# Kernel tuning notes

Hardware: AMD Instinct MI355X
Metric: run time of the kernel (lower is better)

## Reference

```python
import jax, jax.numpy as jnp
import numpy as np

WS = 7
B, Dd, Hh, Wd, C, NH = 1, 28, 28, 28, 384, 12

def _rel_index(ws):
    coords = np.stack(np.meshgrid(np.arange(ws), np.arange(ws), np.arange(ws), indexing='ij'))
    cf = coords.reshape(3, -1)
    rel = (cf[:, :, None] - cf[:, None, :]).transpose(1, 2, 0) + (ws - 1)
    rel[:, :, 0] *= (2 * ws - 1) ** 2
    rel[:, :, 1] *= (2 * ws - 1)
    return rel.sum(-1)  # (ws^3, ws^3)

REL_IDX = _rel_index(WS)

def setup_inputs():
    key = jax.random.key(0)
    ks = jax.random.split(key, 8)
    L = Dd * Hh * Wd
    s = 0.02
    return {
        'skip': jax.random.normal(ks[0], (B, L, C), jnp.float32),
        'x_up': jax.random.normal(ks[1], (B, L, C), jnp.float32),
        'D': Dd, 'H': Hh, 'W': Wd,
        'ln1_g': jnp.ones((C,), jnp.float32), 'ln1_b': jnp.zeros((C,), jnp.float32),
        'kv_w': jax.random.normal(ks[2], (C, 2 * C), jnp.float32) * s,
        'kv_b': jnp.zeros((2 * C,), jnp.float32),
        'rpb': jax.random.normal(ks[3], ((2 * WS - 1) ** 3, NH), jnp.float32) * s,
        'proj_w': jax.random.normal(ks[4], (C, C), jnp.float32) * s,
        'proj_b': jnp.zeros((C,), jnp.float32),
        'ln2_g': jnp.ones((C,), jnp.float32), 'ln2_b': jnp.zeros((C,), jnp.float32),
        'mlp_w1': jax.random.normal(ks[5], (C, 4 * C), jnp.float32) * s,
        'mlp_b1': jnp.zeros((4 * C,), jnp.float32),
        'mlp_w2': jax.random.normal(ks[6], (4 * C, C), jnp.float32) * s,
        'mlp_b2': jnp.zeros((C,), jnp.float32),
    }

def _ln(x, g, b):
    m = jnp.mean(x, -1, keepdims=True)
    v = jnp.mean(jnp.square(x - m), -1, keepdims=True)
    return (x - m) * jax.lax.rsqrt(v + 1e-5) * g + b

def _win_part(x):
    b, d, h, w, c = x.shape
    x = x.reshape(b, d // WS, WS, h // WS, WS, w // WS, WS, c)
    return x.transpose(0, 1, 3, 5, 2, 4, 6, 7).reshape(-1, WS ** 3, c)

def _win_rev(x, b, d, h, w):
    c = x.shape[-1]
    x = x.reshape(b, d // WS, h // WS, w // WS, WS, WS, WS, c)
    return x.transpose(0, 1, 4, 2, 5, 3, 6, 7).reshape(b, d, h, w, c)

def reference(skip, x_up, D, H, W, ln1_g, ln1_b, kv_w, kv_b, rpb, proj_w, proj_b, ln2_g, ln2_b, mlp_w1, mlp_b1, mlp_w2, mlp_b2):
    b, L, c = skip.shape
    x = x_up + skip  # wrapper residual; shortcut of the inner block
    # inner block was built with shift_size=0 -> no cyclic shift, attn_mask unused
    sk = _win_part(_ln(skip, ln1_g, ln1_b).reshape(b, D, H, W, c))   # (nW, N, C) -> K,V source
    qx = _win_part(_ln(x_up, ln1_g, ln1_b).reshape(b, D, H, W, c))   # (nW, N, C) -> Q source
    nW, N, _ = sk.shape
    hd = c // NH
    kv = (sk @ kv_w + kv_b).reshape(nW, N, 2, NH, hd)
    k, v = kv[:, :, 0], kv[:, :, 1]                  # (nW, N, NH, hd)
    q = qx.reshape(nW, N, NH, hd) * (hd ** -0.5)     # no q projection in WindowAttention_kv
    attn = jnp.einsum('wqhd,wkhd->whqk', q, k)
    bias = rpb[REL_IDX.reshape(-1)].reshape(N, N, NH).transpose(2, 0, 1)
    attn = jax.nn.softmax(attn + bias[None], axis=-1)
    o = jnp.einsum('whqk,wkhd->wqhd', attn, v).reshape(nW, N, c)
    o = o @ proj_w + proj_b
    o = _win_rev(o, b, D, H, W).reshape(b, L, c)
    x = x + o
    h1 = jax.nn.gelu(_ln(x, ln2_g, ln2_b) @ mlp_w1 + mlp_b1)
    x = x + h1 @ mlp_w2 + mlp_b2
    return x
```

## Files before the change

### kernel.cpp

```cpp
#include <hip/hip_runtime.h>
#include <hip/hip_bf16.h>
#include <cstdint>

typedef unsigned short u16;
typedef short s16x8 __attribute__((ext_vector_type(8)));
typedef short s16x4 __attribute__((ext_vector_type(4)));
typedef float f32x4 __attribute__((ext_vector_type(4)));

#define C_DIM 384
#define NHEAD 12
#define HD    32
#define NTOK  343
#define NWIN  64
#define LTOT  21952
#define SIDE  28

__device__ __forceinline__ float u2f(u16 u) {
    return __uint_as_float(((unsigned int)u) << 16);
}
__device__ __forceinline__ u16 f2b(float f) {
    unsigned int u = __float_as_uint(f);
    return (u16)((u + 0x7fffu + ((u >> 16) & 1u)) >> 16);
}
__device__ __forceinline__ float exp2_hw(float x) {
    float r;
    asm("v_exp_f32 %0, %1" : "=v"(r) : "v"(x));
    return r;
}
__device__ __forceinline__ unsigned int pk_bf16(float lo, float hi) {
    unsigned int r;
    asm("v_cvt_pk_bf16_f32 %0, %1, %2" : "=v"(r) : "v"(lo), "v"(hi));
    return r;
}
__device__ __forceinline__ float gelu_fast(float x) {
    float e = exp2_hw(-2.3022083f * (x + 0.044715f * x * x * x));
    return x * __builtin_amdgcn_rcpf(1.f + e);
}
__device__ __forceinline__ void gl16(const u16* g, u16* l) {
    __builtin_amdgcn_global_load_lds(
        (const __attribute__((address_space(1))) void*)g,
        (__attribute__((address_space(3))) void*)l, 16, 0, 0);
}

__global__ __launch_bounds__(256) void k_wt(
    const float* __restrict__ W, u16* __restrict__ Wt, int K, int N)
{
    __shared__ float T[64][65];
    int k0 = blockIdx.x * 64, n0 = blockIdx.y * 64;
    int t = threadIdx.x;
    int c = t & 63, rg = t >> 6;
#pragma unroll
    for (int i = 0; i < 16; i++) {
        int r = rg * 16 + i;
        T[r][c] = W[(size_t)(k0 + r) * N + n0 + c];
    }
    __syncthreads();
    int k = t & 63, ng = t >> 6;
#pragma unroll
    for (int i = 0; i < 16; i++) {
        int n = ng * 16 + i;
        Wt[(size_t)(n0 + n) * K + k0 + k] = f2b(T[k][n]);
    }
}

__global__ __launch_bounds__(256) void k_wt_pi(
    const float* __restrict__ W, u16* __restrict__ Wt, int K, int N)
{
    __shared__ float T[64][65];
    int k0 = blockIdx.x * 64, n0 = blockIdx.y * 64;
    int t = threadIdx.x;
    int c = t & 63, rg = t >> 6;
#pragma unroll
    for (int i = 0; i < 16; i++) {
        int r = rg * 16 + i;
        T[r][c] = W[(size_t)(k0 + r) * N + n0 + c];
    }
    __syncthreads();
    int k = t & 63, ng = t >> 6;
    int kg = k0 + k;
    int j = kg & 127, ct = j >> 4, nn = j & 15;
    int kp = (kg & ~127) | ((ct >> 1) << 5) | (nn << 1) | (ct & 1);
#pragma unroll
    for (int i = 0; i < 16; i++) {
        int n = ng * 16 + i;
        Wt[(size_t)(n0 + n) * K + kp] = f2b(T[k][n]);
    }
}

__global__ __launch_bounds__(256) void k_bias(
    const float* __restrict__ rpb, u16* __restrict__ biasPl)
{
    int h = blockIdx.x, q = blockIdx.y;
    int qc = min(q, NTOK - 1);
    int qz = qc / 49, qrem = qc % 49, qy = qrem / 7, qx = qrem % 7;
    int cq = qz * 169 + qy * 13 + qx;
    u16* dst = biasPl + ((size_t)h * 352 + q) * 352;
    for (int k = threadIdx.x; k < 352; k += 256) {
        int kc = min(k, NTOK - 1);
        int kz = kc / 49, krem = kc % 49, ky = krem / 7, kx = krem % 7;
        int ck = kz * 169 + ky * 13 + kx;
        dst[k] = f2b(rpb[(size_t)(cq - ck + 1098) * NHEAD + h] * 1.4426950408889634f);
    }
}

#define QSCALE 0.2550348772f

__global__ __launch_bounds__(256) void k_lnprep(
    const float* __restrict__ skip, const float* __restrict__ xup,
    const float* __restrict__ g, const float* __restrict__ bta,
    u16* __restrict__ skW, u16* __restrict__ qW, u16* __restrict__ res)
{
    int t = blockIdx.x * 4 + (threadIdx.x >> 6);
    int lane = threadIdx.x & 63;
    const float* ps = skip + (size_t)t * C_DIM;
    const float* px = xup + (size_t)t * C_DIM;
    float vs[6], vx[6];
    float s1 = 0.f, s2 = 0.f, x1 = 0.f, x2 = 0.f;
#pragma unroll
    for (int j = 0; j < 6; j++) {
        float a = ps[lane + j * 64];
        float b = px[lane + j * 64];
        vs[j] = a; vx[j] = b;
        s1 += a; s2 += a * a; x1 += b; x2 += b * b;
    }
#pragma unroll
    for (int off = 32; off; off >>= 1) {
        s1 += __shfl_xor(s1, off);
        s2 += __shfl_xor(s2, off);
        x1 += __shfl_xor(x1, off);
        x2 += __shfl_xor(x2, off);
    }
    float ms = s1 * (1.f / 384.f), mx = x1 * (1.f / 384.f);
    float rs = rsqrtf(fmaxf(s2 * (1.f / 384.f) - ms * ms, 0.f) + 1e-5f);
    float rx = rsqrtf(fmaxf(x2 * (1.f / 384.f) - mx * mx, 0.f) + 1e-5f);
    int d = t / 784, rem = t % 784, hh = rem / 28, ww = rem % 28;
    int win = (d / 7) * 16 + (hh / 7) * 4 + (ww / 7);
    int n = (d % 7) * 49 + (hh % 7) * 7 + (ww % 7);
    size_t dst = ((size_t)(win * NTOK + n)) * C_DIM + lane;
    size_t td  = (size_t)t * C_DIM + lane;
#pragma unroll
    for (int j = 0; j < 6; j++) {
        int c = lane + j * 64;
        float gg = g[c], bb = bta[c];
        skW[dst + j * 64] = f2b((vs[j] - ms) * rs * gg + bb);
        qW[dst + j * 64]  = f2b(((vx[j] - mx) * rx * gg + bb) * QSCALE);
        res[td + j * 64]  = f2b(vs[j] + vx[j]);
    }
}

__global__ __launch_bounds__(256) void k_ln2(
    const u16* __restrict__ x2, const float* __restrict__ g,
    const float* __restrict__ bta, u16* __restrict__ lnx)
{
    int t = blockIdx.x * 4 + (threadIdx.x >> 6);
    int lane = threadIdx.x & 63;
    const u16* p = x2 + (size_t)t * C_DIM;
    float v[6];
    float s1 = 0.f, s2 = 0.f;
#pragma unroll
    for (int j = 0; j < 6; j++) {
        float a = u2f(p[lane + j * 64]);
        v[j] = a; s1 += a; s2 += a * a;
    }
#pragma unroll
    for (int off = 32; off; off >>= 1) {
        s1 += __shfl_xor(s1, off);
        s2 += __shfl_xor(s2, off);
    }
    float m = s1 * (1.f / 384.f);
    float r = rsqrtf(fmaxf(s2 * (1.f / 384.f) - m * m, 0.f) + 1e-5f);
    size_t dst = (size_t)t * C_DIM + lane;
#pragma unroll
    for (int j = 0; j < 6; j++) {
        int c = lane + j * 64;
        lnx[dst + j * 64] = f2b((v[j] - m) * r * g[c] + bta[c]);
    }
}

__device__ __forceinline__ void gemm128_gl(
    const u16* __restrict__ A, const u16* __restrict__ Bt, int K, int M,
    int rowBase, int colBase, int tid,
    u16 (*As)[32], u16 (*Bs)[32], f32x4 acc[4][4])
{
    const int sr  = tid >> 2;
    const int scg = (tid & 3) << 3;
    const int lane = tid & 63, wv = tid >> 6;
    const int m16 = lane & 15, quad = lane >> 4;
    const int wr = (wv >> 1) << 6, wc = (wv & 1) << 6;

    int ra0 = min(rowBase + sr, M - 1);
    int ra1 = min(rowBase + 64 + sr, M - 1);
    const u16* pa0 = A + (size_t)ra0 * K + scg;
    const u16* pa1 = A + (size_t)ra1 * K + scg;
    const u16* pb0 = Bt + (size_t)(colBase + sr) * K + scg;
    const u16* pb1 = Bt + (size_t)(colBase + 64 + sr) * K + scg;

    u16* a0d = &As[0][0]  + wv * 512;
    u16* a1d = &As[64][0] + wv * 512;
    u16* b0d = &Bs[0][0]  + wv * 512;
    u16* b1d = &Bs[64][0] + wv * 512;

    gl16(pa0, a0d); gl16(pa1, a1d); gl16(pb0, b0d); gl16(pb1, b1d);
    __syncthreads();

    int buf = 0;
    for (int kk = 0; kk < K; kk += 32) {
        if (kk + 32 < K) {
            int nb = (buf ^ 1) * 4096;
            gl16(pa0 + kk + 32, a0d + nb);
            gl16(pa1 + kk + 32, a1d + nb);
            gl16(pb0 + kk + 32, b0d + nb);
            gl16(pb1 + kk + 32, b1d + nb);
        }
        s16x8 af[4], bf[4];
#pragma unroll
        for (int rt = 0; rt < 4; rt++)
            af[rt] = *(const s16x8*)&As[buf * 128 + wr + rt * 16 + m16][quad * 8];
#pragma unroll
        for (int bt = 0; bt < 4; bt++)
            bf[bt] = *(const s16x8*)&Bs[buf * 128 + wc + bt * 16 + m16][quad * 8];
#pragma unroll
        for (int rt = 0; rt < 4; rt++)
#pragma unroll
        for (int bt = 0; bt < 4; bt++)
            acc[rt][bt] = __builtin_amdgcn_mfma_f32_16x16x32_bf16(af[rt], bf[bt], acc[rt][bt], 0, 0, 0);
        __syncthreads();
        buf ^= 1;
    }
}

__device__ __forceinline__ void gemm64_gl(
    const u16* __restrict__ A, const u16* __restrict__ Bt, int K, int M,
    int rowBase, int colBase, int tid,
    u16 (*As)[32], u16 (*Bs)[32], f32x4 acc[4][2])
{
    const int sr  = tid >> 2;
    const int scg = (tid & 3) << 3;
    const int lane = tid & 63, wv = tid >> 6;
    const int m16 = lane & 15, quad = lane >> 4;
    const int wc = wv << 5;

    int ra = min(rowBase + sr, M - 1);
    const u16* pa  = A + (size_t)ra * K + scg;
    const u16* pb0 = Bt + (size_t)(colBase + sr) * K + scg;
    const u16* pb1 = Bt + (size_t)(colBase + 64 + sr) * K + scg;

    u16* ad  = &As[0][0]  + wv * 512;
    u16* b0d = &Bs[0][0]  + wv * 512;
    u16* b1d = &Bs[64][0] + wv * 512;

    gl16(pa, ad); gl16(pb0, b0d); gl16(pb1, b1d);
    __syncthreads();

    int buf = 0;
    for (int kk = 0; kk < K; kk += 32) {
        if (kk + 32 < K) {
            int nbA = (buf ^ 1) * 2048;
            int nbB = (buf ^ 1) * 4096;
            gl16(pa  + kk + 32, ad  + nbA);
            gl16(pb0 + kk + 32, b0d + nbB);
            gl16(pb1 + kk + 32, b1d + nbB);
        }
        s16x8 af[4], bf[2];
#pragma unroll
        for (int rt = 0; rt < 4; rt++)
            af[rt] = *(const s16x8*)&As[buf * 64 + rt * 16 + m16][quad * 8];
#pragma unroll
        for (int bt = 0; bt < 2; bt++)
            bf[bt] = *(const s16x8*)&Bs[buf * 128 + wc + bt * 16 + m16][quad * 8];
#pragma unroll
        for (int rt = 0; rt < 4; rt++)
#pragma unroll
        for (int bt = 0; bt < 2; bt++)
            acc[rt][bt] = __builtin_amdgcn_mfma_f32_16x16x32_bf16(af[rt], bf[bt], acc[rt][bt], 0, 0, 0);
        __syncthreads();
        buf ^= 1;
    }
}

#define EPI_SETUP \
    int lane = tid & 63, wv = tid >> 6, quad = lane >> 4, n16 = lane & 15;

__global__ __launch_bounds__(256) void k_gemm_kv(
    const u16* __restrict__ A, const u16* __restrict__ Wt, const float* __restrict__ bias,
    u16* __restrict__ Kb, u16* __restrict__ Vb)
{
    __shared__ __align__(16) u16 As[256][32];
    __shared__ __align__(16) u16 Bs[256][32];
    f32x4 acc[4][4] = {};
    int tid = threadIdx.x;
    int rowBase = blockIdx.x * 128, colBase = blockIdx.y * 128;
    gemm128_gl(A, Wt, 384, LTOT, rowBase, colBase, tid, As, Bs, acc);
    EPI_SETUP
    int wr = (wv >> 1) << 6, wc = (wv & 1) << 6;
#pragma unroll
    for (int bt = 0; bt < 4; bt++) {
        int col = colBase + wc + bt * 16 + n16;
        float bcol = bias[col];
        int isv = col >= 384;
        int remc = col - (isv ? 384 : 0);
        int hh = remc >> 5, dd = remc & 31;
#pragma unroll
        for (int rt = 0; rt < 4; rt++)
#pragma unroll
        for (int reg = 0; reg < 4; reg++) {
            int r = rowBase + wr + rt * 16 + quad * 4 + reg;
            if (r < LTOT) {
                int w = r / NTOK, nn = r % NTOK;
                size_t dst = ((size_t)((w * NHEAD + hh) * NTOK + nn)) * HD + dd;
                (isv ? Vb : Kb)[dst] = f2b(acc[rt][bt][reg] + bcol);
            }
        }
    }
}

__global__ __launch_bounds__(256) void k_gemm_proj(
    const u16* __restrict__ A, const u16* __restrict__ Wt, const float* __restrict__ bias,
    const u16* __restrict__ res, u16* __restrict__ x2)
{
    __shared__ __align__(16) u16 As[128][32];
    __shared__ __align__(16) u16 Bs[256][32];
    f32x4 acc[4][2] = {};
    int tid = threadIdx.x;
    int rowBase = blockIdx.x * 64, colBase = blockIdx.y * 128;
    gemm64_gl(A, Wt, 384, LTOT, rowBase, colBase, tid, As, Bs, acc);
    EPI_SETUP
    int wc = wv << 5;
#pragma unroll
    for (int bt = 0; bt < 2; bt++) {
        int col = colBase + wc + bt * 16 + n16;
        float bcol = bias[col];
#pragma unroll
        for (int rt = 0; rt < 4; rt++)
#pragma unroll
        for (int reg = 0; reg < 4; reg++) {
            int r = rowBase + rt * 16 + quad * 4 + reg;
            if (r < LTOT) {
                size_t idx = (size_t)r * C_DIM + col;
                x2[idx] = f2b(acc[rt][bt][reg] + bcol + u2f(res[idx]));
            }
        }
    }
}

__global__ __launch_bounds__(256) void k_gemm_mlp1(
    const u16* __restrict__ A, const u16* __restrict__ Wt, const float* __restrict__ bias,
    u16* __restrict__ h1c, int rowOfs)
{
    __shared__ __align__(16) u16 As[256][32];
    __shared__ __align__(16) u16 Bs[256][32];
    f32x4 acc[4][4] = {};
    int tid = threadIdx.x;
    int rowBase = rowOfs + blockIdx.x * 128, colBase = blockIdx.y * 128;
    gemm128_gl(A, Wt, 384, LTOT, rowBase, colBase, tid, As, Bs, acc);
    EPI_SETUP
    int wr = (wv >> 1) << 6;
#pragma unroll
    for (int p2 = 0; p2 < 2; p2++) {
        int p = (wv & 1) * 2 + p2;
        int col0 = colBase + p * 32 + n16;
        int col1 = col0 + 16;
        float bc0 = bias[col0], bc1 = bias[col1];
        int dcol = colBase + p * 32 + 2 * n16;
#pragma unroll
        for (int rt = 0; rt < 4; rt++)
#pragma unroll
        for (int reg = 0; reg < 4; reg++) {
            int r = rowBase + wr + rt * 16 + quad * 4 + reg;
            if (r < LTOT) {
                size_t rl = (size_t)(r - rowOfs);
                float v0 = gelu_fast(acc[rt][2 * p2][reg] + bc0);
                float v1 = gelu_fast(acc[rt][2 * p2 + 1][reg] + bc1);
                *(unsigned int*)&h1c[rl * 1536 + dcol] = pk_bf16(v0, v1);
            }
        }
    }
}

__global__ __launch_bounds__(256) void k_gemm_mlp2(
    const u16* __restrict__ A, const u16* __restrict__ Wt, const float* __restrict__ bias,
    const u16* __restrict__ x2, float* __restrict__ out, int rowOfs, int chunkRows)
{
    __shared__ __align__(16) u16 As[128][32];
    __shared__ __align__(16) u16 Bs[256][32];
    f32x4 acc[4][2] = {};
    int tid = threadIdx.x;
    int row = blockIdx.x, col = blockIdx.y;
    if (gridDim.x == 343) {
        int v = blockIdx.y * 343 + blockIdx.x;
        int g = v / 24, i = v % 24;
        if (g < 42) { row = g * 8 + (i & 7); col = i >> 3; }
        else        { row = 336 + i % 7;     col = i / 7;  }
    }
    int rowBase = row * 64, colBase = col * 128;
    gemm64_gl(A, Wt, 1536, chunkRows, rowBase, colBase, tid, As, Bs, acc);
    EPI_SETUP
    int wc = wv << 5;
#pragma unroll
    for (int bt = 0; bt < 2; bt++) {
        int c2 = colBase + wc + bt * 16 + n16;
        float bcol = bias[c2];
#pragma unroll
        for (int rt = 0; rt < 4; rt++)
#pragma unroll
        for (int reg = 0; reg < 4; reg++) {
            int rl = rowBase + rt * 16 + quad * 4 + reg;
            int rg = rowOfs + rl;
            if (rl < chunkRows && rg < LTOT) {
                size_t idx = (size_t)rg * C_DIM + c2;
                out[idx] = acc[rt][bt][reg] + bcol + u2f(x2[idx]);
            }
        }
    }
}

#define VP  360
#define PBS 36

__global__ __launch_bounds__(256, 2) void k_attn(
    const u16* __restrict__ qW, const u16* __restrict__ Kb, const u16* __restrict__ Vb,
    const u16* __restrict__ biasPl, u16* __restrict__ oT)
{
    __shared__ __align__(16) u16 Vt[32 * VP];
    __shared__ __align__(16) u16 Pb[4 * 16 * PBS];

    const int h = blockIdx.x, w = blockIdx.y;
    const int tid = threadIdx.x;
    const int lane = tid & 63, wv = tid >> 6;
    const int m16 = lane & 15, quad = lane >> 4;
    const size_t base = ((size_t)(w * NHEAD + h)) * NTOK * HD;
    const u16* Kg = Kb + base;

    for (int t = tid; t < 704; t += 256) {
        int dg = t / 176, rem = t - dg * 176;
        int kb = rem >> 4, j = rem & 15;
        int n0 = kb * 32 + j, n1 = n0 + 16;
        uint4 uA = make_uint4(0, 0, 0, 0), uB = make_uint4(0, 0, 0, 0);
        if (n0 < NTOK) uA = *(const uint4*)(Vb + base + n0 * HD + dg * 8);
        if (n1 < NTOK) uB = *(const uint4*)(Vb + base + n1 * HD + dg * 8);
        int d0 = dg * 8, colu = kb * 32 + 2 * j;
        unsigned int pk0 = (uA.x & 0xffffu) | (uB.x << 16);
        unsigned int pk1 = (uA.x >> 16)     | (uB.x & 0xffff0000u);
        unsigned int pk2 = (uA.y & 0xffffu) | (uB.y << 16);
        unsigned int pk3 = (uA.y >> 16)     | (uB.y & 0xffff0000u);
        unsigned int pk4 = (uA.z & 0xffffu) | (uB.z << 16);
        unsigned int pk5 = (uA.z >> 16)     | (uB.z & 0xffff0000u);
        unsigned int pk6 = (uA.w & 0xffffu) | (uB.w << 16);
        unsigned int pk7 = (uA.w >> 16)     | (uB.w & 0xffff0000u);
        *(unsigned int*)&Vt[(d0 + 0) * VP + colu] = pk0;
        *(unsigned int*)&Vt[(d0 + 1) * VP + colu] = pk1;
        *(unsigned int*)&Vt[(d0 + 2) * VP + colu] = pk2;
        *(unsigned int*)&Vt[(d0 + 3) * VP + colu] = pk3;
        *(unsigned int*)&Vt[(d0 + 4) * VP + colu] = pk4;
        *(unsigned int*)&Vt[(d0 + 5) * VP + colu] = pk5;
        *(unsigned int*)&Vt[(d0 + 6) * VP + colu] = pk6;
        *(unsigned int*)&Vt[(d0 + 7) * VP + colu] = pk7;
    }
    __syncthreads();

    u16* myP = Pb + wv * 16 * PBS;

    for (int qt = wv; qt < 22; qt += 4) {
        int qbase = qt * 16;
        int qrow = min(qbase + m16, NTOK - 1);
        s16x8 qf = *(const s16x8*)(qW + ((size_t)(w * NTOK + qrow)) * C_DIM
                                       + h * HD + quad * 8);
        const u16* bp = biasPl + ((size_t)h * 352 + qbase + quad * 4) * 352;

        f32x4 S0[11], S1[11];
        float mx[4] = {-1e30f, -1e30f, -1e30f, -1e30f};

#pragma unroll
        for (int ks = 0; ks < 11; ks++) {
            int kbase = ks * 32;
            int kt0 = kbase + m16, kt1 = kt0 + 16;
            s16x8 kf0 = *(const s16x8*)(Kg + (size_t)kt0 * HD + quad * 8);
            s16x8 kf1 = *(const s16x8*)(Kg + (size_t)kt1 * HD + quad * 8);
            f32x4 c0, c1;
#pragma unroll
            for (int i = 0; i < 4; i++) {
                c0[i] = u2f(bp[i * 352 + kt0]);
                c1[i] = u2f(bp[i * 352 + kt1]);
            }
            f32x4 sA = __builtin_amdgcn_mfma_f32_16x16x32_bf16(qf, kf0, c0, 0, 0, 0);
            f32x4 sB = __builtin_amdgcn_mfma_f32_16x16x32_bf16(qf, kf1, c1, 0, 0, 0);
            bool k1ok = (ks < 10) || (kt1 < NTOK);
#pragma unroll
            for (int i = 0; i < 4; i++) {
                float sa = sA[i];
                float sb = k1ok ? sB[i] : -1e30f;
                S0[ks][i] = sa;
                S1[ks][i] = sb;
                mx[i] = fmaxf(mx[i], fmaxf(sa, sb));
            }
        }
#pragma unroll
        for (int i = 0; i < 4; i++) {
            float v = mx[i];
            v = fmaxf(v, __shfl_xor(v, 1));
            v = fmaxf(v, __shfl_xor(v, 2));
            v = fmaxf(v, __shfl_xor(v, 4));
            v = fmaxf(v, __shfl_xor(v, 8));
            mx[i] = v;
        }

        f32x4 O0 = {}, O1 = {};
        float l[4] = {};
#pragma unroll
        for (int ks = 0; ks < 11; ks++) {
            int kbase = ks * 32;
#pragma unroll
            for (int i = 0; i < 4; i++) {
                float pa = exp2_hw(S0[ks][i] - mx[i]);
                float pb = exp2_hw(S1[ks][i] - mx[i]);
                l[i] += pa + pb;
                *(unsigned int*)&myP[(quad * 4 + i) * PBS + 2 * m16] = pk_bf16(pa, pb);
            }
            s16x4 plo = *(const s16x4*)&myP[m16 * PBS + quad * 8];
            s16x4 phi = *(const s16x4*)&myP[m16 * PBS + quad * 8 + 4];
            s16x8 pf  = __builtin_shufflevector(plo, phi, 0, 1, 2, 3, 4, 5, 6, 7);
            s16x8 vf0 = *(const s16x8*)&Vt[m16 * VP + kbase + quad * 8];
            s16x8 vf1 = *(const s16x8*)&Vt[(16 + m16) * VP + kbase + quad * 8];
            O0 = __builtin_amdgcn_mfma_f32_16x16x32_bf16(pf, vf0, O0, 0, 0, 0);
            O1 = __builtin_amdgcn_mfma_f32_16x16x32_bf16(pf, vf1, O1, 0, 0, 0);
        }
#pragma unroll
        for (int i = 0; i < 4; i++) {
            float v = l[i];
            v += __shfl_xor(v, 1);
            v += __shfl_xor(v, 2);
            v += __shfl_xor(v, 4);
            v += __shfl_xor(v, 8);
            l[i] = v;
        }

        int wd = w >> 4, wh = (w >> 2) & 3, wwi = w & 3;
#pragma unroll
        for (int i = 0; i < 4; i++) {
            int q = qbase + quad * 4 + i;
            if (q < NTOK) {
                float rl = __builtin_amdgcn_rcpf(l[i]);
                int qz = q / 49, qrem = q % 49, qy = qrem / 7, qx = qrem % 7;
                size_t tok = ((size_t)(wd * 7 + qz) * SIDE + (wh * 7 + qy)) * SIDE
                             + (wwi * 7 + qx);
                u16* op = oT + tok * C_DIM + h * HD;
                op[m16]      = f2b(O0[i] * rl);
                op[16 + m16] = f2b(O1[i] * rl);
            }
        }
    }
}

extern "C" void kernel_launch(void* const* d_in, const int* in_sizes, int n_in,
                              void* d_out, int out_size, void* d_ws, size_t ws_size,
                              hipStream_t stream)
{
    const float* skip = (const float*)d_in[0];
    const float* xup  = (const float*)d_in[1];
    const float* ln1g = (const float*)d_in[5];
    const float* ln1b = (const float*)d_in[6];
    const float* kvw  = (const float*)d_in[7];
    const float* kvb  = (const float*)d_in[8];
    const float* rpb  = (const float*)d_in[9];
    const float* pw   = (const float*)d_in[10];
    const float* pb   = (const float*)d_in[11];
    const float* ln2g = (const float*)d_in[12];
    const float* ln2b = (const float*)d_in[13];
    const float* w1   = (const float*)d_in[14];
    const float* b1   = (const float*)d_in[15];
    const float* w2   = (const float*)d_in[16];
    const float* b2   = (const float*)d_in[17];
    float* out = (float*)d_out;

    char* ws = (char*)d_ws;
    const size_t BUFB = (size_t)LTOT * C_DIM * 2;
    const size_t WTB  = 589824 + 294912 + 1179648 + 1179648;
    const size_t BIASB = (size_t)NHEAD * 352 * 352 * 2;
    u16* skW = (u16*)(ws);
    u16* qW  = (u16*)(ws + BUFB);
    u16* Kb  = (u16*)(ws + 2 * BUFB);
    u16* Vb  = (u16*)(ws + 3 * BUFB);
    u16* oT  = (u16*)(ws);
    u16* x2  = (u16*)(ws + BUFB);
    u16* lnx = (u16*)(ws + 2 * BUFB);
    char* wt = ws + 4 * BUFB;
    u16* kvWt = (u16*)(wt);
    u16* pWt  = (u16*)(wt + 589824);
    u16* w1t  = (u16*)(wt + 589824 + 294912);
    u16* w2t  = (u16*)(wt + 589824 + 294912 + 1179648);
    u16* biasPl = (u16*)(wt + WTB);
    u16* res  = (u16*)d_out;

    const size_t used = 4 * BUFB + WTB + BIASB;
    const size_t blkBytes = 128 * 1536 * 2;
    size_t tailCap = (ws_size > used) ? (ws_size - used) / blkBytes : 0;
    int chunkBlocks;
    u16* h1c;
    if (tailCap >= 43) {
        chunkBlocks = tailCap < 172 ? (int)tailCap : 172;
        h1c = (u16*)(ws + used);
    } else {
        chunkBlocks = 42;
        h1c = (u16*)(ws + 3 * BUFB);
    }

    k_wt<<<dim3(6, 12), 256, 0, stream>>>(kvw, kvWt, 384, 768);
    k_wt<<<dim3(6, 6),  256, 0, stream>>>(pw,  pWt,  384, 384);
    k_wt<<<dim3(6, 24), 256, 0, stream>>>(w1,  w1t,  384, 1536);
    k_wt_pi<<<dim3(24, 6), 256, 0, stream>>>(w2, w2t, 1536, 384);
    k_bias<<<dim3(NHEAD, 352), 256, 0, stream>>>(rpb, biasPl);

    k_lnprep<<<LTOT / 4, 256, 0, stream>>>(skip, xup, ln1g, ln1b, skW, qW, res);
    k_gemm_kv<<<dim3(172, 6), 256, 0, stream>>>(skW, kvWt, kvb, Kb, Vb);
    k_attn<<<dim3(NHEAD, NWIN), 256, 0, stream>>>(qW, Kb, Vb, biasPl, oT);
    k_gemm_proj<<<dim3(343, 3), 256, 0, stream>>>(oT, pWt, pb, res, x2);
    k_ln2<<<LTOT / 4, 256, 0, stream>>>(x2, ln2g, ln2b, lnx);
    for (int b0 = 0; b0 < 172; b0 += chunkBlocks) {
        int nb = (172 - b0) < chunkBlocks ? (172 - b0) : chunkBlocks;
        int rowOfs = b0 * 128;
        int chunkRows = nb * 128;
        if (rowOfs + chunkRows > LTOT) chunkRows = LTOT - rowOfs;
        int nb64 = (chunkRows + 63) / 64;
        k_gemm_mlp1<<<dim3(nb, 12), 256, 0, stream>>>(lnx, w1t, b1, h1c, rowOfs);
        k_gemm_mlp2<<<dim3(nb64, 3), 256, 0, stream>>>(h1c, w2t, b2, x2, out, rowOfs, chunkRows);
    }
}
```

Measured before the change: 410.9 us.

## Deepen gemm64 pipeline to 4-stage LDS ring with vmcnt-based waits

Replaces the double-buffered gemm64 main loop used by the projection and MLP2 GEMMs with a 4-slot LDS ring that keeps two K-tiles of global-to-LDS loads in flight. Explicit s_waitcnt vmcnt counts and a single s_barrier per iteration replace the two __syncthreads per step, with sched_barrier fences to hold instruction order. The aim is to hide global load latency and cut synchronisation cost. The cost is double the LDS footprint per block, which may lower occupancy, plus correctness that now depends on the hand-counted outstanding-load numbers.

```diff
diff --git a/kernel.cpp b/kernel.cpp
--- a/kernel.cpp
+++ b/kernel.cpp
@@ -229,7 +229,7 @@
     }
 }
 
-__device__ __forceinline__ void gemm64_gl(
+__device__ __forceinline__ void gemm64_cnt(
     const u16* __restrict__ A, const u16* __restrict__ Bt, int K, int M,
     int rowBase, int colBase, int tid,
     u16 (*As)[32], u16 (*Bs)[32], f32x4 acc[4][2])
@@ -249,33 +249,42 @@
     u16* b0d = &Bs[0][0]  + wv * 512;
     u16* b1d = &Bs[64][0] + wv * 512;
 
-    gl16(pa, ad); gl16(pb0, b0d); gl16(pb1, b1d);
-    __syncthreads();
-
-    int buf = 0;
-    for (int kk = 0; kk < K; kk += 32) {
-        if (kk + 32 < K) {
-            int nbA = (buf ^ 1) * 2048;
-            int nbB = (buf ^ 1) * 4096;
-            gl16(pa  + kk + 32, ad  + nbA);
-            gl16(pb0 + kk + 32, b0d + nbB);
-            gl16(pb1 + kk + 32, b1d + nbB);
-        }
+    const int NP = K >> 5;
+    gl16(pa,      ad);        gl16(pb0,      b0d);        gl16(pb1,      b1d);
+    gl16(pa + 32, ad + 2048); gl16(pb0 + 32, b0d + 4096); gl16(pb1 + 32, b1d + 4096);
+    __builtin_amdgcn_sched_barrier(0);
+
+    for (int p = 0; p < NP; ++p) {
+        int b = p & 3;
+        if (p + 2 < NP) {
+            int nb = (p + 2) & 3;
+            int ko = (p + 2) << 5;
+            gl16(pa  + ko, ad  + nb * 2048);
+            gl16(pb0 + ko, b0d + nb * 4096);
+            gl16(pb1 + ko, b1d + nb * 4096);
+            asm volatile("s_waitcnt vmcnt(6)");
+        } else if (p + 2 == NP) {
+            asm volatile("s_waitcnt vmcnt(3)");
+        } else {
+            asm volatile("s_waitcnt vmcnt(0)");
+        }
+        __builtin_amdgcn_s_barrier();
+        __builtin_amdgcn_sched_barrier(0);
         s16x8 af[4], bf[2];
 #pragma unroll
         for (int rt = 0; rt < 4; rt++)
-            af[rt] = *(const s16x8*)&As[buf * 64 + rt * 16 + m16][quad * 8];
+            af[rt] = *(const s16x8*)&As[b * 64 + rt * 16 + m16][quad * 8];
 #pragma unroll
         for (int bt = 0; bt < 2; bt++)
-            bf[bt] = *(const s16x8*)&Bs[buf * 128 + wc + bt * 16 + m16][quad * 8];
+            bf[bt] = *(const s16x8*)&Bs[b * 128 + wc + bt * 16 + m16][quad * 8];
 #pragma unroll
         for (int rt = 0; rt < 4; rt++)
 #pragma unroll
         for (int bt = 0; bt < 2; bt++)
             acc[rt][bt] = __builtin_amdgcn_mfma_f32_16x16x32_bf16(af[rt], bf[bt], acc[rt][bt], 0, 0, 0);
-        __syncthreads();
-        buf ^= 1;
-    }
+        __builtin_amdgcn_sched_barrier(0);
+    }
+    __builtin_amdgcn_s_barrier();
 }
 
 #define EPI_SETUP \
@@ -318,12 +327,12 @@
     const u16* __restrict__ A, const u16* __restrict__ Wt, const float* __restrict__ bias,
     const u16* __restrict__ res, u16* __restrict__ x2)
 {
-    __shared__ __align__(16) u16 As[128][32];
-    __shared__ __align__(16) u16 Bs[256][32];
+    __shared__ __align__(16) u16 As[256][32];
+    __shared__ __align__(16) u16 Bs[512][32];
     f32x4 acc[4][2] = {};
     int tid = threadIdx.x;
     int rowBase = blockIdx.x * 64, colBase = blockIdx.y * 128;
-    gemm64_gl(A, Wt, 384, LTOT, rowBase, colBase, tid, As, Bs, acc);
+    gemm64_cnt(A, Wt, 384, LTOT, rowBase, colBase, tid, As, Bs, acc);
     EPI_SETUP
     int wc = wv << 5;
 #pragma unroll
@@ -381,8 +390,8 @@
     const u16* __restrict__ A, const u16* __restrict__ Wt, const float* __restrict__ bias,
     const u16* __restrict__ x2, float* __restrict__ out, int rowOfs, int chunkRows)
 {
-    __shared__ __align__(16) u16 As[128][32];
-    __shared__ __align__(16) u16 Bs[256][32];
+    __shared__ __align__(16) u16 As[256][32];
+    __shared__ __align__(16) u16 Bs[512][32];
     f32x4 acc[4][2] = {};
     int tid = threadIdx.x;
     int row = blockIdx.x, col = blockIdx.y;
@@ -393,7 +402,7 @@
         else        { row = 336 + i % 7;     col = i / 7;  }
     }
     int rowBase = row * 64, colBase = col * 128;
-    gemm64_gl(A, Wt, 1536, chunkRows, rowBase, colBase, tid, As, Bs, acc);
+    gemm64_cnt(A, Wt, 1536, chunkRows, rowBase, colBase, tid, As, Bs, acc);
     EPI_SETUP
     int wc = wv << 5;
 #pragma unroll
```

Result: slower. 430.8 us (+4.8%).
